# Performance work log

Hardware: AMD Instinct MI355X
Metric: run time of the kernel (lower is better)

Reference implementation:

```python
import jax, jax.numpy as jnp
import numpy as np

N = 50000
E = 1600000
IN = 128
HID = 64
HEADS = 2
OUT = 32
NEG_SLOPE = 0.2  # PyG GATConv default negative_slope


def _gat_conv(x, edge_index, edge_attr, W, a_src, a_dst, W_e, a_e, bias, heads, out_ch, concat):
    """Faithful PyG GATConv with edge_dim, add_self_loops=True (fill_value='mean')."""
    n = x.shape[0]
    src, dst = edge_index[0], edge_index[1]
    # self-loop edge_attr = per-node mean of incoming edge attrs (PyG fill_value='mean')
    ones = jnp.ones((src.shape[0],), x.dtype)
    deg = jax.ops.segment_sum(ones, dst, num_segments=n)
    loop_attr = jax.ops.segment_sum(edge_attr, dst, num_segments=n) / jnp.maximum(deg, 1.0)[:, None]
    loop = jnp.arange(n)
    src = jnp.concatenate([src, loop])
    dst = jnp.concatenate([dst, loop])
    ea = jnp.concatenate([edge_attr, loop_attr], axis=0)  # [E+N, 1]
    # node / edge projections
    h = (x @ W).reshape(n, heads, out_ch)                 # [N, H, C]
    al_src = jnp.sum(h * a_src, axis=-1)                  # [N, H]
    al_dst = jnp.sum(h * a_dst, axis=-1)                  # [N, H]
    he = (ea @ W_e).reshape(-1, heads, out_ch)            # [E+N, H, C]
    al_e = jnp.sum(he * a_e, axis=-1)                     # [E+N, H]
    logits = jax.nn.leaky_relu(al_src[src] + al_dst[dst] + al_e, NEG_SLOPE)
    # segment softmax over destination nodes
    m = jax.ops.segment_max(logits, dst, num_segments=n)  # [N, H]
    p = jnp.exp(logits - m[dst])
    denom = jax.ops.segment_sum(p, dst, num_segments=n)
    alpha = p / (denom[dst] + 1e-16)                      # [E+N, H]
    # weighted scatter-aggregate of source messages
    out = jax.ops.segment_sum(alpha[:, :, None] * h[src], dst, num_segments=n)  # [N, H, C]
    out = out.reshape(n, heads * out_ch) if concat else out.mean(axis=1)
    return out + bias


def setup_inputs() -> dict:
    key = jax.random.key(0)
    ks = jax.random.split(key, 16)
    x = jax.random.normal(ks[0], (N, IN), dtype=jnp.float32)
    edge_index = jax.random.randint(ks[1], (2, E), 0, N)
    edge_weight = jax.random.uniform(ks[2], (E, 1), dtype=jnp.float32)
    s1 = 1.0 / np.sqrt(IN)
    W1 = jax.random.normal(ks[3], (IN, HEADS * HID), dtype=jnp.float32) * s1
    att_src1 = jax.random.normal(ks[4], (HEADS, HID), dtype=jnp.float32) * 0.1
    att_dst1 = jax.random.normal(ks[5], (HEADS, HID), dtype=jnp.float32) * 0.1
    We1 = jax.random.normal(ks[6], (1, HEADS * HID), dtype=jnp.float32) * 0.5
    att_e1 = jax.random.normal(ks[7], (HEADS, HID), dtype=jnp.float32) * 0.1
    b1 = jnp.zeros((HEADS * HID,), dtype=jnp.float32)
    s2 = 1.0 / np.sqrt(HEADS * HID)
    W2 = jax.random.normal(ks[8], (HEADS * HID, OUT), dtype=jnp.float32) * s2
    att_src2 = jax.random.normal(ks[9], (1, OUT), dtype=jnp.float32) * 0.1
    att_dst2 = jax.random.normal(ks[10], (1, OUT), dtype=jnp.float32) * 0.1
    We2 = jax.random.normal(ks[11], (1, OUT), dtype=jnp.float32) * 0.5
    att_e2 = jax.random.normal(ks[12], (1, OUT), dtype=jnp.float32) * 0.1
    b2 = jnp.zeros((OUT,), dtype=jnp.float32)
    return {"x": x, "edge_index": edge_index, "edge_weight": edge_weight,
            "W1": W1, "att_src1": att_src1, "att_dst1": att_dst1, "We1": We1, "att_e1": att_e1, "b1": b1,
            "W2": W2, "att_src2": att_src2, "att_dst2": att_dst2, "We2": We2, "att_e2": att_e2, "b2": b2}


def reference(x, edge_index, edge_weight, W1, att_src1, att_dst1, We1, att_e1, b1,
              W2, att_src2, att_dst2, We2, att_e2, b2):
    h = _gat_conv(x, edge_index, edge_weight, W1, att_src1, att_dst1, We1, att_e1, b1,
                  HEADS, HID, True)
    h = jax.nn.elu(h)
    return _gat_conv(h, edge_index, edge_weight, W2, att_src2, att_dst2, We2, att_e2, b2,
                     1, OUT, False)
```

## Files before the change

kernel.cpp:

```cpp
#include <hip/hip_runtime.h>
#include <hip/hip_fp16.h>

#define NEG_SLOPE 0.2f
#define NBUK 8
#define NPB  6272
#define NFINE 512
#define FPN  98
#define BCAP (2048*104)
#define FCAP 4096
#define EPT 8

__device__ __forceinline__ float wredsum(float v){
  #pragma unroll
  for (int k=32;k;k>>=1) v += __shfl_xor(v,k,64);
  return v;
}

__global__ void k_init(int* __restrict__ tails, int* __restrict__ tails2,
                       const float* __restrict__ We1, const float* __restrict__ ae1,
                       const float* __restrict__ We2, const float* __restrict__ ae2,
                       float* __restrict__ cst){
  int t = threadIdx.x;
  if (t < NBUK) tails[t] = 0;
  if (t < NFINE) tails2[t] = 0;
  if (t == 0){
    float c0 = 0.f, c1 = 0.f, c2 = 0.f;
    for (int k = 0; k < 64; k++){ c0 += We1[k]*ae1[k]; c1 += We1[64+k]*ae1[64+k]; }
    for (int k = 0; k < 32; k++){ c2 += We2[k]*ae2[k]; }
    cst[0] = c0; cst[1] = c1; cst[2] = c2;
  }
}

__global__ __launch_bounds__(256) void k_pA(const int* __restrict__ ei,
                        const float* __restrict__ ew,
                        uint2* __restrict__ bbuf, int* __restrict__ tails, int E_){
  __shared__ uint2 sb[2048];
  __shared__ unsigned char sfb[2048];
  __shared__ int scnt[NBUK], sbase[NBUK], sgb[NBUK];
  const int t = threadIdx.x;
  const int e0 = blockIdx.x*2048;
  if (t < NBUK) scnt[t] = 0;
  __syncthreads();
  int mb[EPT]; uint2 me[EPT]; bool ok[EPT];
  #pragma unroll
  for (int u = 0; u < EPT; u++){
    int e = e0 + u*256 + t;
    ok[u] = (e < E_); mb[u] = 0;
    if (ok[u]){
      int dst = ei[E_ + e], src = ei[e];
      float wv = ew[e];
      mb[u] = dst / NPB;
      me[u] = make_uint2(((unsigned)dst << 16) | (unsigned)src, __float_as_uint(wv));
      atomicAdd(&scnt[mb[u]], 1);
    }
  }
  __syncthreads();
  if (t == 0){ int run = 0;
    #pragma unroll
    for (int j = 0; j < NBUK; j++){ sbase[j] = run; run += scnt[j]; } }
  __syncthreads();
  if (t < NBUK) scnt[t] = 0;
  __syncthreads();
  #pragma unroll
  for (int u = 0; u < EPT; u++)
    if (ok[u]){
      int p = sbase[mb[u]] + atomicAdd(&scnt[mb[u]], 1);
      sb[p] = me[u]; sfb[p] = (unsigned char)mb[u];
    }
  __syncthreads();
  if (t < NBUK) sgb[t] = atomicAdd(&tails[t], scnt[t]);
  __syncthreads();
  int total = sbase[NBUK-1] + scnt[NBUK-1];
  for (int p = t; p < total; p += 256){
    int bb = sfb[p];
    int g = sgb[bb] + (p - sbase[bb]);
    if (g < BCAP) bbuf[(size_t)bb*BCAP + g] = sb[p];
  }
}

__global__ __launch_bounds__(256) void k_pB1(const uint2* __restrict__ bbuf,
                        const int* __restrict__ tails,
                        uint2* __restrict__ fbuf, int* __restrict__ tails2){
  __shared__ uint2 sb[2048];
  __shared__ unsigned char sfb[2048];
  __shared__ int scnt[64], sbase[64], sgb[64];
  const int coarse = blockIdx.x & 7, chunk = blockIdx.x >> 3;
  const int cnt = min(tails[coarse], BCAP);
  const int t = threadIdx.x;
  const int i0 = chunk*2048;
  if (i0 >= cnt) return;
  if (t < 64) scnt[t] = 0;
  __syncthreads();
  int fl[EPT]; uint2 me[EPT]; bool ok[EPT];
  #pragma unroll
  for (int u = 0; u < EPT; u++){
    int i = i0 + u*256 + t;
    ok[u] = (i < cnt); fl[u] = 0;
    if (ok[u]){
      me[u] = bbuf[(size_t)coarse*BCAP + i];
      int dst = (int)(me[u].x >> 16);
      fl[u] = dst/FPN - coarse*64;
      atomicAdd(&scnt[fl[u]], 1);
    }
  }
  __syncthreads();
  if (t == 0){ int run = 0;
    for (int j = 0; j < 64; j++){ sbase[j] = run; run += scnt[j]; } }
  __syncthreads();
  if (t < 64) scnt[t] = 0;
  __syncthreads();
  #pragma unroll
  for (int u = 0; u < EPT; u++)
    if (ok[u]){
      int p = sbase[fl[u]] + atomicAdd(&scnt[fl[u]], 1);
      sb[p] = me[u]; sfb[p] = (unsigned char)fl[u];
    }
  __syncthreads();
  if (t < 64) sgb[t] = atomicAdd(&tails2[coarse*64 + t], scnt[t]);
  __syncthreads();
  int total = sbase[63] + scnt[63];
  for (int p = t; p < total; p += 256){
    int f = sfb[p];
    int g = sgb[f] + (p - sbase[f]);
    if (g < FCAP) fbuf[(size_t)(coarse*64 + f)*FCAP + g] = sb[p];
  }
}

__global__ __launch_bounds__(256) void k_pB2(const uint2* __restrict__ fbuf,
                        const int* __restrict__ tails2,
                        unsigned* __restrict__ csr, int* __restrict__ rp,
                        int* __restrict__ dg, int N_){
  __shared__ unsigned csr4[FCAP];
  __shared__ int scnt[100], sbase[100], sfill[100];
  const int f = blockIdx.x;
  const int cnt = min(tails2[f], FCAP);
  const int t = threadIdx.x;
  const int n0 = f*FPN;
  if (t < 100){ scnt[t] = 0; sfill[t] = 0; }
  __syncthreads();
  const uint2* srcb = fbuf + (size_t)f*FCAP;
  for (int i = t; i < cnt; i += 256){
    int dst = (int)(srcb[i].x >> 16);
    atomicAdd(&scnt[dst - n0], 1);
  }
  __syncthreads();
  if (t == 0){ int run = 0;
    for (int j = 0; j < FPN; j++){ sbase[j] = run; run += scnt[j]; } }
  __syncthreads();
  for (int i = t; i < cnt; i += 256){
    uint2 e = srcb[i];
    int loc = (int)(e.x >> 16) - n0;
    int pos = sbase[loc] + atomicAdd(&sfill[loc], 1);
    unsigned h = (unsigned)__half_as_ushort(__float2half(__uint_as_float(e.y)));
    csr4[pos] = (h << 16) | (e.x & 0xFFFFu);
  }
  __syncthreads();
  const int base = f*FCAP;
  for (int i = t; i < cnt; i += 256) csr[base + i] = csr4[i];
  if (t < FPN){
    int n = n0 + t;
    if (n < N_){ rp[n] = base + sbase[t]; dg[n] = scnt[t]; }
  }
}

__global__ __launch_bounds__(256) void k_gemm1(
    const float* __restrict__ x, const float* __restrict__ W,
    const float* __restrict__ pa_s, const float* __restrict__ pa_d,
    __half* __restrict__ h1h, float* __restrict__ alsrc, float* __restrict__ aldst, int N_)
{
  __shared__ float ws[64*128];
  __shared__ float xs[16][128];
  const int t = threadIdx.x;
  const int row0 = blockIdx.x*16;
  const float4* x4 = (const float4*)(x + (size_t)row0*128);
  float4* xs4 = (float4*)xs;
  for (int i = t; i < 512; i += 256){
    int r = i >> 5;
    xs4[i] = (row0 + r < N_) ? x4[i] : make_float4(0.f,0.f,0.f,0.f);
  }
  const int c = t & 127, rh = t >> 7;
  float acc[8];
  #pragma unroll
  for (int u = 0; u < 8; u++) acc[u] = 0.f;
  const float4* W4 = (const float4*)W;
  float4* ws4 = (float4*)ws;
  for (int kt = 0; kt < 2; kt++){
    __syncthreads();
    for (int i = t; i < 2048; i += 256) ws4[i] = W4[kt*2048 + i];
    __syncthreads();
    #pragma unroll 8
    for (int k = 0; k < 64; k++){
      float wv = ws[k*128 + c];
      #pragma unroll
      for (int u = 0; u < 8; u++) acc[u] = fmaf(xs[rh*8+u][kt*64 + k], wv, acc[u]);
    }
  }
  #pragma unroll
  for (int u = 0; u < 8; u++){
    int row = row0 + rh*8 + u;
    if (row < N_) h1h[(size_t)row*128 + c] = __float2half(acc[u]);
  }
  __syncthreads();
  #pragma unroll
  for (int u = 0; u < 8; u++) xs[rh*8+u][c] = acc[u];
  __syncthreads();
  if (t < 32){
    int rr = t >> 1, hh = t & 1;
    int orow = row0 + rr;
    if (orow < N_){
      float ps = 0.f, pd = 0.f;
      for (int c2 = 0; c2 < 64; c2++){
        float hv = xs[rr][hh*64 + c2];
        ps = fmaf(hv, pa_s[hh*64 + c2], ps);
        pd = fmaf(hv, pa_d[hh*64 + c2], pd);
      }
      alsrc[orow*2 + hh] = ps;
      aldst[orow*2 + hh] = pd;
    }
  }
}

__global__ __launch_bounds__(256) void k_layer1(
  const int* __restrict__ rp, const int* __restrict__ dg,
  const unsigned* __restrict__ csr,
  const float* __restrict__ alsrc, const float* __restrict__ aldst,
  const __half* __restrict__ h1h, const float* __restrict__ b1,
  const float* __restrict__ cst, float* __restrict__ hx, int N_)
{
  int wid = (blockIdx.x*256 + threadIdx.x) >> 6;
  int lane = threadIdx.x & 63;
  if (wid >= N_) return;
  const int n = wid;
  const int deg = dg[n];
  const int p0 = rp[n];
  const float ce0 = cst[0], ce1 = cst[1];
  const float2 adv = *(const float2*)&aldst[2*n];
  const int quad = lane >> 4;
  const int ch8 = (lane & 15) * 8;
  const int head = ch8 >> 6;
  float acc[8] = {0.f,0.f,0.f,0.f,0.f,0.f,0.f,0.f};
  float sum0 = 0.f, sum1 = 0.f, wsum = 0.f;

  for (int base = 0; base < deg; base += 64){
    int i = base + lane;
    float pp0 = 0.f, pp1 = 0.f; int s = 0;
    if (i < deg){
      unsigned pk = csr[p0 + i];
      s = (int)(pk & 0xFFFFu);
      float ea = __half2float(__ushort_as_half((unsigned short)(pk >> 16)));
      wsum += ea;
      float2 av = *(const float2*)&alsrc[2*s];
      float l0 = av.x + adv.x + ea*ce0;
      float l1 = av.y + adv.y + ea*ce1;
      l0 = (l0 > 0.f) ? l0 : NEG_SLOPE*l0;
      l1 = (l1 > 0.f) ? l1 : NEG_SLOPE*l1;
      pp0 = __expf(l0); pp1 = __expf(l1);
    }
    sum0 += pp0; sum1 += pp1;
    int lim = min(64, deg - base);
    for (int jb = 0; jb < lim; jb += 4){
      int j  = jb + quad;
      int jc = (j < lim) ? j : 0;
      int   sj = __shfl(s,   jc, 64);
      float q0 = __shfl(pp0, jc, 64);
      float q1 = __shfl(pp1, jc, 64);
      float q  = head ? q1 : q0;
      if (j < lim){
        uint4 hv = *(const uint4*)(h1h + (size_t)sj*128 + ch8);
        const half2* hp = (const half2*)&hv;
        #pragma unroll
        for (int u = 0; u < 4; u++){
          float2 fv = __half22float2(hp[u]);
          acc[2*u]   = fmaf(q, fv.x, acc[2*u]);
          acc[2*u+1] = fmaf(q, fv.y, acc[2*u+1]);
        }
      }
    }
  }
  sum0 = wredsum(sum0); sum1 = wredsum(sum1); wsum = wredsum(wsum);

  float mean = wsum / fmaxf((float)deg, 1.0f);
  float2 avs = *(const float2*)&alsrc[2*n];
  float ls0 = avs.x + adv.x + mean*ce0;
  float ls1 = avs.y + adv.y + mean*ce1;
  ls0 = (ls0 > 0.f) ? ls0 : NEG_SLOPE*ls0;
  ls1 = (ls1 > 0.f) ? ls1 : NEG_SLOPE*ls1;
  float ps0 = __expf(ls0), ps1 = __expf(ls1);
  sum0 += ps0; sum1 += ps1;

  #pragma unroll
  for (int u = 0; u < 8; u++){
    acc[u] += __shfl_xor(acc[u], 16, 64);
    acc[u] += __shfl_xor(acc[u], 32, 64);
  }

  if (lane < 16){
    float qs = head ? ps1 : ps0;
    uint4 hv = *(const uint4*)(h1h + (size_t)n*128 + ch8);
    const half2* hp = (const half2*)&hv;
    #pragma unroll
    for (int u = 0; u < 4; u++){
      float2 fv = __half22float2(hp[u]);
      acc[2*u]   = fmaf(qs, fv.x, acc[2*u]);
      acc[2*u+1] = fmaf(qs, fv.y, acc[2*u+1]);
    }
    float inv = head ? 1.f/(sum1 + 1e-16f) : 1.f/(sum0 + 1e-16f);
    float4 b0 = *(const float4*)&b1[ch8];
    float4 b4 = *(const float4*)&b1[ch8 + 4];
    float vv[8];
    #pragma unroll
    for (int u = 0; u < 8; u++){
      float bv = (u < 4) ? (&b0.x)[u] : (&b4.x)[u-4];
      float v = acc[u]*inv + bv;
      vv[u] = (v > 0.f) ? v : expm1f(v);
    }
    *(float4*)&hx[(size_t)n*128 + ch8]     = make_float4(vv[0],vv[1],vv[2],vv[3]);
    *(float4*)&hx[(size_t)n*128 + ch8 + 4] = make_float4(vv[4],vv[5],vv[6],vv[7]);
  }
}

__global__ __launch_bounds__(256) void k_gemm2(
  const float* __restrict__ hx, const float* __restrict__ W2,
  const float* __restrict__ as2, const float* __restrict__ ad2,
  __half* __restrict__ h2h, float* __restrict__ alsrc2, float* __restrict__ aldst2, int N_)
{
  __shared__ float ws_[128*32];
  __shared__ float hs[8][32];
  int t = threadIdx.x;
  const float4* W4 = (const float4*)W2;
  float4* s4 = (float4*)ws_;
  for (int i = t; i < 1024; i += 256) s4[i] = W4[i];
  __syncthreads();
  int gid = blockIdx.x*256 + t;
  int n = gid >> 5, c = gid & 31;
  float acc = 0.f;
  if (n < N_){
    const float4* xr = (const float4*)(hx + (size_t)n*128);
    #pragma unroll
    for (int k4 = 0; k4 < 32; k4++){
      float4 xv = xr[k4];
      acc = fmaf(xv.x, ws_[(k4*4+0)*32 + c], acc);
      acc = fmaf(xv.y, ws_[(k4*4+1)*32 + c], acc);
      acc = fmaf(xv.z, ws_[(k4*4+2)*32 + c], acc);
      acc = fmaf(xv.w, ws_[(k4*4+3)*32 + c], acc);
    }
    h2h[(size_t)n*32 + c] = __float2half(acc);
  }
  hs[t>>5][c] = acc;
  __syncthreads();
  if (t < 8){
    int nn = blockIdx.x*8 + t;
    if (nn < N_){
      float ps = 0.f, pd = 0.f;
      for (int c2 = 0; c2 < 32; c2++){
        float hv = hs[t][c2];
        ps = fmaf(hv, as2[c2], ps);
        pd = fmaf(hv, ad2[c2], pd);
      }
      alsrc2[nn] = ps;
      aldst2[nn] = pd;
    }
  }
}

__global__ __launch_bounds__(256) void k_layer2(
  const int* __restrict__ rp, const int* __restrict__ dg,
  const unsigned* __restrict__ csr,
  const float* __restrict__ alsrc2, const float* __restrict__ aldst2,
  const __half* __restrict__ h2h, const float* __restrict__ b2,
  const float* __restrict__ cst, float* __restrict__ out, int N_)
{
  int wid = (blockIdx.x*256 + threadIdx.x) >> 6;
  int lane = threadIdx.x & 63;
  if (wid >= N_) return;
  const int n = wid;
  const int deg = dg[n];
  const int p0 = rp[n];
  const float ce2 = cst[2];
  const float adn = aldst2[n];
  const int oct = lane >> 3;
  const int ch4 = (lane & 7) * 4;
  float acc[4] = {0.f,0.f,0.f,0.f};
  float sum = 0.f, wsum = 0.f;

  for (int base = 0; base < deg; base += 64){
    int i = base + lane;
    float pp = 0.f; int s = 0;
    if (i < deg){
      unsigned pk = csr[p0 + i];
      s = (int)(pk & 0xFFFFu);
      float ea = __half2float(__ushort_as_half((unsigned short)(pk >> 16)));
      wsum += ea;
      float l = alsrc2[s] + ea*ce2 + adn;
      l = (l > 0.f) ? l : NEG_SLOPE*l;
      pp = __expf(l);
    }
    sum += pp;
    int lim = min(64, deg - base);
    for (int jb = 0; jb < lim; jb += 8){
      int j  = jb + oct;
      int jc = (j < lim) ? j : 0;
      float q  = __shfl(pp, jc, 64);
      int   sj = __shfl(s,  jc, 64);
      if (j < lim){
        uint2 hv = *(const uint2*)(h2h + (size_t)sj*32 + ch4);
        const half2* hp = (const half2*)&hv;
        float2 f0 = __half22float2(hp[0]);
        float2 f1 = __half22float2(hp[1]);
        acc[0] = fmaf(q, f0.x, acc[0]);
        acc[1] = fmaf(q, f0.y, acc[1]);
        acc[2] = fmaf(q, f1.x, acc[2]);
        acc[3] = fmaf(q, f1.y, acc[3]);
      }
    }
  }
  sum = wredsum(sum); wsum = wredsum(wsum);

  float mean = wsum / fmaxf((float)deg, 1.0f);
  float ls = alsrc2[n] + mean*ce2 + adn;
  ls = (ls > 0.f) ? ls : NEG_SLOPE*ls;
  float ps = __expf(ls);
  sum += ps;

  #pragma unroll
  for (int u = 0; u < 4; u++){
    acc[u] += __shfl_xor(acc[u],  8, 64);
    acc[u] += __shfl_xor(acc[u], 16, 64);
    acc[u] += __shfl_xor(acc[u], 32, 64);
  }
  if (lane < 8){
    uint2 hv = *(const uint2*)(h2h + (size_t)n*32 + ch4);
    const half2* hp = (const half2*)&hv;
    float2 f0 = __half22float2(hp[0]);
    float2 f1 = __half22float2(hp[1]);
    acc[0] = fmaf(ps, f0.x, acc[0]);
    acc[1] = fmaf(ps, f0.y, acc[1]);
    acc[2] = fmaf(ps, f1.x, acc[2]);
    acc[3] = fmaf(ps, f1.y, acc[3]);
    float inv = 1.f/(sum + 1e-16f);
    float4 bv = *(const float4*)&b2[ch4];
    float4 o;
    o.x = acc[0]*inv + bv.x;
    o.y = acc[1]*inv + bv.y;
    o.z = acc[2]*inv + bv.z;
    o.w = acc[3]*inv + bv.w;
    *(float4*)&out[(size_t)n*32 + ch4] = o;
  }
}

extern "C" void kernel_launch(void* const* d_in, const int* in_sizes, int n_in,
                              void* d_out, int out_size, void* d_ws, size_t ws_size,
                              hipStream_t stream)
{
  const float* x   = (const float*)d_in[0];
  const int*   ei  = (const int*)d_in[1];
  const float* ew  = (const float*)d_in[2];
  const float* W1  = (const float*)d_in[3];
  const float* as1 = (const float*)d_in[4];
  const float* ad1 = (const float*)d_in[5];
  const float* We1 = (const float*)d_in[6];
  const float* ae1 = (const float*)d_in[7];
  const float* b1  = (const float*)d_in[8];
  const float* W2  = (const float*)d_in[9];
  const float* as2 = (const float*)d_in[10];
  const float* ad2 = (const float*)d_in[11];
  const float* We2 = (const float*)d_in[12];
  const float* ae2 = (const float*)d_in[13];
  const float* b2  = (const float*)d_in[14];
  const int N_ = in_sizes[0] / 128;
  const int E_ = in_sizes[1] / 2;

  char* w = (char*)d_ws;
  size_t o = 0;
  auto alloc = [&](size_t b){ size_t r = o; o = (o + b + 255) & ~(size_t)255; return r; };
  size_t o_tail  = alloc(NBUK*4);
  size_t o_tail2 = alloc(NFINE*4);
  size_t o_cst   = alloc(64);
  size_t o_bbuf  = alloc((size_t)NBUK*BCAP*8);
  size_t o_fbuf  = alloc((size_t)NFINE*FCAP*8);
  size_t o_csr   = alloc((size_t)NFINE*FCAP*4);
  size_t o_rp    = alloc((size_t)N_*4);
  size_t o_dg    = alloc((size_t)N_*4);
  size_t o_h1    = alloc((size_t)N_*128*2);
  size_t o_hx    = alloc((size_t)N_*128*4);
  size_t o_h2    = alloc((size_t)N_*32*2);
  size_t o_als1  = alloc((size_t)N_*8);
  size_t o_ald1  = alloc((size_t)N_*8);
  size_t o_als2  = alloc((size_t)N_*4);
  size_t o_ald2  = alloc((size_t)N_*4);

  int*      tails = (int*)(w+o_tail);
  int*      tails2= (int*)(w+o_tail2);
  float*    cst   = (float*)(w+o_cst);
  uint2*    bbuf  = (uint2*)(w+o_bbuf);
  uint2*    fbuf  = (uint2*)(w+o_fbuf);
  unsigned* csr   = (unsigned*)(w+o_csr);
  int*      rp    = (int*)(w+o_rp);
  int*      dg    = (int*)(w+o_dg);
  __half*   h1h   = (__half*)(w+o_h1);
  float*    hx    = (float*)(w+o_hx);
  __half*   h2h   = (__half*)(w+o_h2);
  float*    als1  = (float*)(w+o_als1);
  float*    ald1  = (float*)(w+o_ald1);
  float*    als2  = (float*)(w+o_als2);
  float*    ald2  = (float*)(w+o_ald2);
  float*    out   = (float*)d_out;

  int nA  = (E_ + 2047) / 2048;
  int nB1 = (BCAP / 2048) * NBUK;

  k_init<<<1, 512, 0, stream>>>(tails, tails2, We1, ae1, We2, ae2, cst);
  k_pA<<<nA, 256, 0, stream>>>(ei, ew, bbuf, tails, E_);
  k_pB1<<<nB1, 256, 0, stream>>>(bbuf, tails, fbuf, tails2);
  k_pB2<<<NFINE, 256, 0, stream>>>(fbuf, tails2, csr, rp, dg, N_);
  k_gemm1<<<(N_+15)/16, 256, 0, stream>>>(x, W1, as1, ad1, h1h, als1, ald1, N_);
  k_layer1<<<(N_+3)/4, 256, 0, stream>>>(rp, dg, csr, als1, ald1, h1h, b1, cst, hx, N_);
  k_gemm2<<<((N_*32)+255)/256, 256, 0, stream>>>(hx, W2, as2, ad2, h2h, als2, ald2, N_);
  k_layer2<<<(N_+3)/4, 256, 0, stream>>>(rp, dg, csr, als2, ald2, h2h, b2, cst, out, N_);
}
```

Measured before the change: 221.8 us.

## Fuse edge bucketing with gemm1 and fold gemm2 into layer1 epilogue

```diff
diff --git a/kernel.cpp b/kernel.cpp
--- a/kernel.cpp
+++ b/kernel.cpp
@@ -31,50 +31,113 @@
   }
 }
 
-__global__ __launch_bounds__(256) void k_pA(const int* __restrict__ ei,
-                        const float* __restrict__ ew,
-                        uint2* __restrict__ bbuf, int* __restrict__ tails, int E_){
-  __shared__ uint2 sb[2048];
-  __shared__ unsigned char sfb[2048];
+__global__ __launch_bounds__(256) void k_pA_gemm1(
+    const int* __restrict__ ei, const float* __restrict__ ew,
+    uint2* __restrict__ bbuf, int* __restrict__ tails,
+    const float* __restrict__ x, const float* __restrict__ W,
+    const float* __restrict__ pa_s, const float* __restrict__ pa_d,
+    __half* __restrict__ h1h, float* __restrict__ alsrc, float* __restrict__ aldst,
+    int N_, int E_, int nG, int nTot)
+{
+  __shared__ float ws[64*128];
+  __shared__ float xs[16][128];
   __shared__ int scnt[NBUK], sbase[NBUK], sgb[NBUK];
+  const int b = blockIdx.x;
   const int t = threadIdx.x;
-  const int e0 = blockIdx.x*2048;
-  if (t < NBUK) scnt[t] = 0;
-  __syncthreads();
-  int mb[EPT]; uint2 me[EPT]; bool ok[EPT];
-  #pragma unroll
-  for (int u = 0; u < EPT; u++){
-    int e = e0 + u*256 + t;
-    ok[u] = (e < E_); mb[u] = 0;
-    if (ok[u]){
-      int dst = ei[E_ + e], src = ei[e];
-      float wv = ew[e];
-      mb[u] = dst / NPB;
-      me[u] = make_uint2(((unsigned)dst << 16) | (unsigned)src, __float_as_uint(wv));
-      atomicAdd(&scnt[mb[u]], 1);
-    }
-  }
-  __syncthreads();
-  if (t == 0){ int run = 0;
+  const size_t gb = (size_t)b * (size_t)nG / (size_t)nTot;
+  const bool is_g = ((size_t)(b+1) * (size_t)nG / (size_t)nTot) > gb;
+
+  if (!is_g){
+    uint2* sb = (uint2*)ws;
+    unsigned char* sfb = (unsigned char*)(ws + 4096);
+    const int e0 = (b - (int)gb) * 2048;
+    if (t < NBUK) scnt[t] = 0;
+    __syncthreads();
+    int mb[EPT]; uint2 me[EPT]; bool ok[EPT];
     #pragma unroll
-    for (int j = 0; j < NBUK; j++){ sbase[j] = run; run += scnt[j]; } }
-  __syncthreads();
-  if (t < NBUK) scnt[t] = 0;
-  __syncthreads();
-  #pragma unroll
-  for (int u = 0; u < EPT; u++)
-    if (ok[u]){
-      int p = sbase[mb[u]] + atomicAdd(&scnt[mb[u]], 1);
-      sb[p] = me[u]; sfb[p] = (unsigned char)mb[u];
-    }
-  __syncthreads();
-  if (t < NBUK) sgb[t] = atomicAdd(&tails[t], scnt[t]);
-  __syncthreads();
-  int total = sbase[NBUK-1] + scnt[NBUK-1];
-  for (int p = t; p < total; p += 256){
-    int bb = sfb[p];
-    int g = sgb[bb] + (p - sbase[bb]);
-    if (g < BCAP) bbuf[(size_t)bb*BCAP + g] = sb[p];
+    for (int u = 0; u < EPT; u++){
+      int e = e0 + u*256 + t;
+      ok[u] = (e < E_); mb[u] = 0;
+      if (ok[u]){
+        int dst = ei[E_ + e], src = ei[e];
+        float wv = ew[e];
+        mb[u] = dst / NPB;
+        me[u] = make_uint2(((unsigned)dst << 16) | (unsigned)src, __float_as_uint(wv));
+        atomicAdd(&scnt[mb[u]], 1);
+      }
+    }
+    __syncthreads();
+    if (t == 0){ int run = 0;
+      #pragma unroll
+      for (int j = 0; j < NBUK; j++){ sbase[j] = run; run += scnt[j]; } }
+    __syncthreads();
+    if (t < NBUK) scnt[t] = 0;
+    __syncthreads();
+    #pragma unroll
+    for (int u = 0; u < EPT; u++)
+      if (ok[u]){
+        int p = sbase[mb[u]] + atomicAdd(&scnt[mb[u]], 1);
+        sb[p] = me[u]; sfb[p] = (unsigned char)mb[u];
+      }
+    __syncthreads();
+    if (t < NBUK) sgb[t] = atomicAdd(&tails[t], scnt[t]);
+    __syncthreads();
+    int total = sbase[NBUK-1] + scnt[NBUK-1];
+    for (int p = t; p < total; p += 256){
+      int bb = sfb[p];
+      int g = sgb[bb] + (p - sbase[bb]);
+      if (g < BCAP) bbuf[(size_t)bb*BCAP + g] = sb[p];
+    }
+    return;
+  }
+
+  const int row0 = (int)gb * 16;
+  if (row0 >= N_) return;
+  const float4* x4 = (const float4*)(x + (size_t)row0*128);
+  float4* xs4 = (float4*)xs;
+  for (int i = t; i < 512; i += 256){
+    int r = i >> 5;
+    xs4[i] = (row0 + r < N_) ? x4[i] : make_float4(0.f,0.f,0.f,0.f);
+  }
+  const int c = t & 127, rh = t >> 7;
+  float acc[8];
+  #pragma unroll
+  for (int u = 0; u < 8; u++) acc[u] = 0.f;
+  const float4* W4 = (const float4*)W;
+  float4* ws4 = (float4*)ws;
+  for (int kt = 0; kt < 2; kt++){
+    __syncthreads();
+    for (int i = t; i < 2048; i += 256) ws4[i] = W4[kt*2048 + i];
+    __syncthreads();
+    #pragma unroll 8
+    for (int k = 0; k < 64; k++){
+      float wv = ws[k*128 + c];
+      #pragma unroll
+      for (int u = 0; u < 8; u++) acc[u] = fmaf(xs[rh*8+u][kt*64 + k], wv, acc[u]);
+    }
+  }
+  #pragma unroll
+  for (int u = 0; u < 8; u++){
+    int row = row0 + rh*8 + u;
+    if (row < N_) h1h[(size_t)row*128 + c] = __float2half(acc[u]);
+  }
+  __syncthreads();
+  #pragma unroll
+  for (int u = 0; u < 8; u++) xs[rh*8+u][c] = acc[u];
+  __syncthreads();
+  if (t < 32){
+    int rr = t >> 1, hh = t & 1;
+    int orow = row0 + rr;
+    if (orow < N_){
+      float ps = 0.f, pd = 0.f;
+      for (int c2 = 0; c2 < 64; c2++){
+        float hv = xs[rr][hh*64 + c2];
+        ps = fmaf(hv, pa_s[hh*64 + c2], ps);
+        pd = fmaf(hv, pa_d[hh*64 + c2], pd);
+      }
+      alsrc[orow*2 + hh] = ps;
+      aldst[orow*2 + hh] = pd;
+    }
   }
 }
 
@@ -163,74 +226,33 @@
   }
 }
 
-__global__ __launch_bounds__(256) void k_gemm1(
-    const float* __restrict__ x, const float* __restrict__ W,
-    const float* __restrict__ pa_s, const float* __restrict__ pa_d,
-    __half* __restrict__ h1h, float* __restrict__ alsrc, float* __restrict__ aldst, int N_)
-{
-  __shared__ float ws[64*128];
-  __shared__ float xs[16][128];
-  const int t = threadIdx.x;
-  const int row0 = blockIdx.x*16;
-  const float4* x4 = (const float4*)(x + (size_t)row0*128);
-  float4* xs4 = (float4*)xs;
-  for (int i = t; i < 512; i += 256){
-    int r = i >> 5;
-    xs4[i] = (row0 + r < N_) ? x4[i] : make_float4(0.f,0.f,0.f,0.f);
-  }
-  const int c = t & 127, rh = t >> 7;
-  float acc[8];
-  #pragma unroll
-  for (int u = 0; u < 8; u++) acc[u] = 0.f;
-  const float4* W4 = (const float4*)W;
-  float4* ws4 = (float4*)ws;
-  for (int kt = 0; kt < 2; kt++){
-    __syncthreads();
-    for (int i = t; i < 2048; i += 256) ws4[i] = W4[kt*2048 + i];
-    __syncthreads();
-    #pragma unroll 8
-    for (int k = 0; k < 64; k++){
-      float wv = ws[k*128 + c];
-      #pragma unroll
-      for (int u = 0; u < 8; u++) acc[u] = fmaf(xs[rh*8+u][kt*64 + k], wv, acc[u]);
-    }
-  }
-  #pragma unroll
-  for (int u = 0; u < 8; u++){
-    int row = row0 + rh*8 + u;
-    if (row < N_) h1h[(size_t)row*128 + c] = __float2half(acc[u]);
-  }
-  __syncthreads();
-  #pragma unroll
-  for (int u = 0; u < 8; u++) xs[rh*8+u][c] = acc[u];
-  __syncthreads();
-  if (t < 32){
-    int rr = t >> 1, hh = t & 1;
-    int orow = row0 + rr;
-    if (orow < N_){
-      float ps = 0.f, pd = 0.f;
-      for (int c2 = 0; c2 < 64; c2++){
-        float hv = xs[rr][hh*64 + c2];
-        ps = fmaf(hv, pa_s[hh*64 + c2], ps);
-        pd = fmaf(hv, pa_d[hh*64 + c2], pd);
-      }
-      alsrc[orow*2 + hh] = ps;
-      aldst[orow*2 + hh] = pd;
-    }
-  }
-}
-
 __global__ __launch_bounds__(256) void k_layer1(
   const int* __restrict__ rp, const int* __restrict__ dg,
   const unsigned* __restrict__ csr,
   const float* __restrict__ alsrc, const float* __restrict__ aldst,
   const __half* __restrict__ h1h, const float* __restrict__ b1,
-  const float* __restrict__ cst, float* __restrict__ hx, int N_)
+  const float* __restrict__ cst, const float* __restrict__ W2,
+  const float* __restrict__ as2, const float* __restrict__ ad2,
+  __half* __restrict__ h2h, float* __restrict__ alsrc2, float* __restrict__ aldst2,
+  int N_)
 {
-  int wid = (blockIdx.x*256 + threadIdx.x) >> 6;
-  int lane = threadIdx.x & 63;
+  __shared__ float W2s[128*32];
+  __shared__ float sas[32], sad[32];
+  __shared__ float hxs[4][128];
+  const int t = threadIdx.x;
+  {
+    const float4* W4 = (const float4*)W2;
+    float4* s4 = (float4*)W2s;
+    for (int i = t; i < 1024; i += 256) s4[i] = W4[i];
+    if (t < 32){ sas[t] = as2[t]; sad[t] = ad2[t]; }
+  }
+  __syncthreads();
+
+  int wid = (blockIdx.x*256 + t) >> 6;
+  int lane = t & 63;
   if (wid >= N_) return;
   const int n = wid;
+  const int wv_ = t >> 6;
   const int deg = dg[n];
   const int p0 = rp[n];
   const float ce0 = cst[0], ce1 = cst[1];
@@ -314,53 +336,23 @@
       float v = acc[u]*inv + bv;
       vv[u] = (v > 0.f) ? v : expm1f(v);
     }
-    *(float4*)&hx[(size_t)n*128 + ch8]     = make_float4(vv[0],vv[1],vv[2],vv[3]);
-    *(float4*)&hx[(size_t)n*128 + ch8 + 4] = make_float4(vv[4],vv[5],vv[6],vv[7]);
-  }
-}
-
-__global__ __launch_bounds__(256) void k_gemm2(
-  const float* __restrict__ hx, const float* __restrict__ W2,
-  const float* __restrict__ as2, const float* __restrict__ ad2,
-  __half* __restrict__ h2h, float* __restrict__ alsrc2, float* __restrict__ aldst2, int N_)
-{
-  __shared__ float ws_[128*32];
-  __shared__ float hs[8][32];
-  int t = threadIdx.x;
-  const float4* W4 = (const float4*)W2;
-  float4* s4 = (float4*)ws_;
-  for (int i = t; i < 1024; i += 256) s4[i] = W4[i];
-  __syncthreads();
-  int gid = blockIdx.x*256 + t;
-  int n = gid >> 5, c = gid & 31;
-  float acc = 0.f;
-  if (n < N_){
-    const float4* xr = (const float4*)(hx + (size_t)n*128);
-    #pragma unroll
-    for (int k4 = 0; k4 < 32; k4++){
-      float4 xv = xr[k4];
-      acc = fmaf(xv.x, ws_[(k4*4+0)*32 + c], acc);
-      acc = fmaf(xv.y, ws_[(k4*4+1)*32 + c], acc);
-      acc = fmaf(xv.z, ws_[(k4*4+2)*32 + c], acc);
-      acc = fmaf(xv.w, ws_[(k4*4+3)*32 + c], acc);
-    }
-    h2h[(size_t)n*32 + c] = __float2half(acc);
-  }
-  hs[t>>5][c] = acc;
-  __syncthreads();
-  if (t < 8){
-    int nn = blockIdx.x*8 + t;
-    if (nn < N_){
-      float ps = 0.f, pd = 0.f;
-      for (int c2 = 0; c2 < 32; c2++){
-        float hv = hs[t][c2];
-        ps = fmaf(hv, as2[c2], ps);
-        pd = fmaf(hv, ad2[c2], pd);
-      }
-      alsrc2[nn] = ps;
-      aldst2[nn] = pd;
-    }
-  }
+    *(float4*)&hxs[wv_][ch8]     = make_float4(vv[0],vv[1],vv[2],vv[3]);
+    *(float4*)&hxs[wv_][ch8 + 4] = make_float4(vv[4],vv[5],vv[6],vv[7]);
+  }
+  __builtin_amdgcn_wave_barrier();
+
+  const int c2 = lane & 31, kh = lane >> 5;
+  const float* hb = hxs[wv_] + kh*64;
+  float a2 = 0.f;
+  #pragma unroll 16
+  for (int k = 0; k < 64; k++)
+    a2 = fmaf(hb[k], W2s[(kh*64 + k)*32 + c2], a2);
+  a2 += __shfl_xor(a2, 32, 64);
+  float ps = a2 * sas[c2], pd = a2 * sad[c2];
+  #pragma unroll
+  for (int k2 = 16; k2; k2 >>= 1){ ps += __shfl_xor(ps, k2, 64); pd += __shfl_xor(pd, k2, 64); }
+  if (lane < 32) h2h[(size_t)n*32 + c2] = __float2half(a2);
+  if (lane == 0){ alsrc2[n] = ps; aldst2[n] = pd; }
 }
 
 __global__ __launch_bounds__(256) void k_layer2(
@@ -482,7 +474,6 @@
   size_t o_rp    = alloc((size_t)N_*4);
   size_t o_dg    = alloc((size_t)N_*4);
   size_t o_h1    = alloc((size_t)N_*128*2);
-  size_t o_hx    = alloc((size_t)N_*128*4);
   size_t o_h2    = alloc((size_t)N_*32*2);
   size_t o_als1  = alloc((size_t)N_*8);
   size_t o_ald1  = alloc((size_t)N_*8);
@@ -498,7 +489,6 @@
   int*      rp    = (int*)(w+o_rp);
   int*      dg    = (int*)(w+o_dg);
   __half*   h1h   = (__half*)(w+o_h1);
-  float*    hx    = (float*)(w+o_hx);
   __half*   h2h   = (__half*)(w+o_h2);
   float*    als1  = (float*)(w+o_als1);
   float*    ald1  = (float*)(w+o_ald1);
@@ -506,15 +496,17 @@
   float*    ald2  = (float*)(w+o_ald2);
   float*    out   = (float*)d_out;
 
-  int nA  = (E_ + 2047) / 2048;
+  int nB  = (E_ + 2047) / 2048;
+  int nG  = (N_ + 15) / 16;
+  int nTot = nB + nG;
   int nB1 = (BCAP / 2048) * NBUK;
 
   k_init<<<1, 512, 0, stream>>>(tails, tails2, We1, ae1, We2, ae2, cst);
-  k_pA<<<nA, 256, 0, stream>>>(ei, ew, bbuf, tails, E_);
+  k_pA_gemm1<<<nTot, 256, 0, stream>>>(ei, ew, bbuf, tails, x, W1, as1, ad1,
+                                       h1h, als1, ald1, N_, E_, nG, nTot);
   k_pB1<<<nB1, 256, 0, stream>>>(bbuf, tails, fbuf, tails2);
   k_pB2<<<NFINE, 256, 0, stream>>>(fbuf, tails2, csr, rp, dg, N_);
-  k_gemm1<<<(N_+15)/16, 256, 0, stream>>>(x, W1, as1, ad1, h1h, als1, ald1, N_);
-  k_layer1<<<(N_+3)/4, 256, 0, stream>>>(rp, dg, csr, als1, ald1, h1h, b1, cst, hx, N_);
-  k_gemm2<<<((N_*32)+255)/256, 256, 0, stream>>>(hx, W2, as2, ad2, h2h, als2, ald2, N_);
+  k_layer1<<<(N_+3)/4, 256, 0, stream>>>(rp, dg, csr, als1, ald1, h1h, b1, cst,
+                                         W2, as2, ad2, h2h, als2, ald2, N_);
   k_layer2<<<(N_+3)/4, 256, 0, stream>>>(rp, dg, csr, als2, ald2, h2h, b2, cst, out, N_);
 }
```

Result: faster. 202.2 us (-8.8%).
